# Optimization experiments

Measured on AMD Instinct MI355X. Metric: run time of the kernel, lower is better.

## Reference

```python
import jax, jax.numpy as jnp
import numpy as np

H1 = 768
H2 = 768
B, LQ, LK = 8, 1024, 1024


def setup_inputs() -> dict:
    key = jax.random.key(0)
    ks = jax.random.split(key, 12)
    s1 = 1.0 / np.sqrt(H1)
    s2 = 1.0 / np.sqrt(H2)
    # weights stored as [in, out] (equivalent to torch Linear weight.T)
    return {
        "tensor1": jax.random.normal(ks[0], (B, LQ, H1), jnp.float32),
        "tensor2": jax.random.normal(ks[1], (B, LK, H2), jnp.float32),
        "Wq": jax.random.uniform(ks[2], (3, H1, H2), jnp.float32, -s1, s1),
        "bq": jax.random.uniform(ks[3], (3, H2), jnp.float32, -s1, s1),
        "Wk": jax.random.uniform(ks[4], (3, H2, H2), jnp.float32, -s2, s2),
        "bk": jax.random.uniform(ks[5], (3, H2), jnp.float32, -s2, s2),
        "Wv": jax.random.uniform(ks[6], (3, H2, H2), jnp.float32, -s2, s2),
        "bv": jax.random.uniform(ks[7], (3, H2), jnp.float32, -s2, s2),
        "Wp": jax.random.uniform(ks[8], (3 * H2, H2), jnp.float32, -1.0 / np.sqrt(3 * H2), 1.0 / np.sqrt(3 * H2)),
        "bp": jax.random.uniform(ks[9], (H2,), jnp.float32, -1.0 / np.sqrt(3 * H2), 1.0 / np.sqrt(3 * H2)),
    }


def reference(tensor1, tensor2, Wq, bq, Wk, bk, Wv, bv, Wp, bp):
    # Three independent cross-attention heads, stacked on leading axis h=3.
    q = jnp.einsum("bqd,hde->hbqe", tensor1, Wq) + bq[:, None, None, :]  # [3,B,LQ,H2]
    k = jnp.einsum("bkd,hde->hbke", tensor2, Wk) + bk[:, None, None, :]  # [3,B,LK,H2]
    v = jnp.einsum("bkd,hde->hbke", tensor2, Wv) + bv[:, None, None, :]  # [3,B,LK,H2]
    scores = jnp.einsum("hbqe,hbke->hbqk", q, k)  # NOTE: no 1/sqrt(d) scaling, per original
    weights = jax.nn.softmax(scores, axis=-1)
    ctx = jnp.einsum("hbqk,hbke->hbqe", weights, v)  # [3,B,LQ,H2]
    # concat heads along feature dim -> [B,LQ,3*H2]
    multi = jnp.transpose(ctx, (1, 2, 0, 3)).reshape(ctx.shape[1], ctx.shape[2], -1)
    # project_multihead: ReLU then Linear
    return jax.nn.relu(multi) @ Wp + bp
```

## Files before the change

### kernel.cpp

```cpp
#include <hip/hip_runtime.h>
#include <hip/hip_bf16.h>


typedef _Float16 f16;
typedef __attribute__((ext_vector_type(8))) _Float16 f16x8;
typedef __attribute__((ext_vector_type(4))) float f32x4;
typedef __attribute__((ext_vector_type(4))) short s16x4;
typedef __attribute__((ext_vector_type(8))) short s16x8;

#define DI __device__ __forceinline__

DI short f2hs(float f){
  f16 h = (f16)f;
  return __builtin_bit_cast(short, h);
}

DI f32x4 mfma16(f16x8 a, f16x8 b, f32x4 c){
  return __builtin_amdgcn_mfma_f32_16x16x32_f16(a, b, c, 0, 0, 0);
}

#define GLL16(gp, lp) __builtin_amdgcn_global_load_lds( \
    (const __attribute__((address_space(1))) unsigned int*)(gp), \
    (__attribute__((address_space(3))) unsigned int*)(lp), 16, 0, 0)

__global__ void pre_fused_kernel(
    const float* __restrict__ t1, const float* __restrict__ t2,
    short* __restrict__ t1b, short* __restrict__ t2b,
    const float* __restrict__ Wq, const float* __restrict__ Wk,
    short* __restrict__ Mt,
    const float* __restrict__ Wv, const float* __restrict__ Wp,
    short* __restrict__ WvT, short* __restrict__ WpT,
    const float* __restrict__ bq, float* __restrict__ wvb)
{
  __shared__ short As[8192];
  __shared__ short Bs[8192];
  __shared__ float tile[32][33];
  int bid = blockIdx.x;
  const int tid = threadIdx.x;

  if (bid < 108){
    const int h = bid / 36, rem = bid % 36;
    const int m0 = (rem / 6) * 128, n0 = (rem % 6) * 128;
    const float* A  = Wq + (long)h*768*768;
    const float* Bt = Wk + (long)h*768*768;
    const int wave = tid>>6, lane = tid&63;
    const int wm = wave>>1, wn = wave&1;
    const int fl = lane&15, fq = lane>>4;
    const int srow = lane>>2, sl = lane&3;
    const int gco = (sl ^ ((srow>>1)&3))*8;
    const int rs  = (fq ^ ((fl>>1)&3))*8;

    f32x4 vz = {0.f,0.f,0.f,0.f};
    f32x4 acc[4][4];
    #pragma unroll
    for (int i=0;i<4;i++)
      #pragma unroll
      for (int j=0;j<4;j++) acc[i][j] = vz;

    for (int kk=0; kk<768; kk+=64){
      __syncthreads();
      #pragma unroll
      for (int c=0;c<2;c++)
        #pragma unroll
        for (int r=0;r<2;r++){
          const int row = r*64 + wave*16 + srow;
          const int gc  = kk + c*32 + gco;
          const float* pa = A  + (long)(m0+row)*768 + gc;
          const float* pb = Bt + (long)(n0+row)*768 + gc;
          f32x4 a0 = *(const f32x4*)pa, a1 = *(const f32x4*)(pa+4);
          f32x4 b0 = *(const f32x4*)pb, b1 = *(const f32x4*)(pb+4);
          s16x8 ha, hb;
          #pragma unroll
          for (int e=0;e<4;e++){ ha[e]=f2hs(a0[e]); ha[4+e]=f2hs(a1[e]);
                                 hb[e]=f2hs(b0[e]); hb[4+e]=f2hs(b1[e]); }
          *(s16x8*)(As + c*4096 + row*32 + sl*8) = ha;
          *(s16x8*)(Bs + c*4096 + row*32 + sl*8) = hb;
        }
      __syncthreads();
      #pragma unroll
      for (int c=0;c<2;c++){
        f16x8 a[4];
        #pragma unroll
        for (int i=0;i<4;i++) a[i] = *(const f16x8*)(As + c*4096 + (wm*64+i*16+fl)*32 + rs);
        #pragma unroll
        for (int j=0;j<4;j++){
          f16x8 b = *(const f16x8*)(Bs + c*4096 + (wn*64+j*16+fl)*32 + rs);
          #pragma unroll
          for (int i=0;i<4;i++) acc[i][j] = mfma16(a[i], b, acc[i][j]);
        }
      }
    }

    short* outp = Mt + (long)h*768*768;
    #pragma unroll
    for (int j=0;j<4;j++){
      int col = n0 + wn*64 + j*16 + fl;
      #pragma unroll
      for (int i=0;i<4;i++){
        int row = m0 + wm*64 + i*16 + fq*4;
        s16x4 pack;
        #pragma unroll
        for (int r=0;r<4;r++) pack[r] = f2hs(acc[i][j][r]);
        *(s16x4*)(outp + (long)col*768 + row) = pack;
      }
    }
    return;
  }
  bid -= 108;
  if (bid < 24){
    const int h = bid / 8, chunk = bid % 8;
    const int wave = tid>>6, lane = tid&63;
    const float* bql = bq + h*768 + lane*12;
    float bv[12];
    #pragma unroll
    for (int e=0;e<12;e++) bv[e] = bql[e];
    for (int r = 0; r < 24; r++){
      int d = chunk*96 + r*4 + wave;
      const float* row = Wk + ((long)h*768 + d)*768 + lane*12;
      float s = 0.f;
      #pragma unroll
      for (int e=0;e<12;e++) s += row[e] * bv[e];
      s += __shfl_xor(s, 1);
      s += __shfl_xor(s, 2);
      s += __shfl_xor(s, 4);
      s += __shfl_xor(s, 8);
      s += __shfl_xor(s, 16);
      s += __shfl_xor(s, 32);
      if (lane == 0) wvb[h*768 + d] = s;
    }
    return;
  }
  bid -= 24;
  if (bid < 3456){
    const int bz = bid / 1728, rem = bid % 1728;
    const int by = rem / 24, bx = rem % 24;
    const float* in; short* out; int R, r0;
    if (bz == 0){
      int hd = by / 24;
      in = Wv + (long)hd*768*768; out = WvT + (long)hd*768*768;
      R = 768; r0 = (by % 24) * 32;
    } else {
      in = Wp; out = WpT; R = 2304; r0 = by * 32;
    }
    int c0 = bx * 32;
    int tx = tid & 31, ty = tid >> 5;
    #pragma unroll
    for (int k=0;k<4;k++)
      tile[ty + k*8][tx] = in[(long)(r0 + ty + k*8) * 768 + c0 + tx];
    __syncthreads();
    #pragma unroll
    for (int k=0;k<4;k++)
      out[(long)(c0 + ty + k*8) * R + r0 + tx] = f2hs(tile[tx][ty + k*8]);
    return;
  }
  bid -= 3456;
  {
    int i = bid*256 + tid;
    const float* in = (i < 1572864) ? t1 : t2;
    short* out = (i < 1572864) ? t1b : t2b;
    int j = (i < 1572864) ? i : i - 1572864;
    f32x4 v = ((const f32x4*)in)[j];
    s16x4 o;
    o[0]=f2hs(v[0]); o[1]=f2hs(v[1]); o[2]=f2hs(v[2]); o[3]=f2hs(v[3]);
    ((s16x4*)out)[j] = o;
  }
}

DI void gemm_tile64(const short* __restrict__ A, const short* __restrict__ Bt, int K,
                    int m0, int n0, short* As, short* Bs, f32x4 (&acc)[4][4])
{
  const int tid = threadIdx.x, wave = tid>>6, lane = tid&63;
  const int wm = wave>>1, wn = wave&1;
  const int fl = lane&15, fq = lane>>4;
  const int srow = lane>>2;
  const int scol = ((lane&3) ^ ((lane>>3)&3))*8;
  const int rs   = (fq ^ ((fl>>1)&3))*8;
  for (int kk=0; kk<K; kk+=64){
    __syncthreads();
    #pragma unroll
    for (int c=0;c<2;c++)
      #pragma unroll
      for (int r=0;r<2;r++){
        const int rb = r*64 + wave*16;
        GLL16(A  + (long)(m0+rb+srow)*K + kk + c*32 + scol, As + c*4096 + rb*32);
        GLL16(Bt + (long)(n0+rb+srow)*K + kk + c*32 + scol, Bs + c*4096 + rb*32);
      }
    __syncthreads();
    #pragma unroll
    for (int c=0;c<2;c++){
      f16x8 a[4];
      #pragma unroll
      for (int i=0;i<4;i++) a[i] = *(const f16x8*)(As + c*4096 + (wm*64+i*16+fl)*32 + rs);
      #pragma unroll
      for (int j=0;j<4;j++){
        f16x8 b = *(const f16x8*)(Bs + c*4096 + (wn*64+j*16+fl)*32 + rs);
        #pragma unroll
        for (int i=0;i<4;i++) acc[i][j] = mfma16(a[i], b, acc[i][j]);
      }
    }
  }
}

__global__ __launch_bounds__(256,2) void gemm_gv_kernel(
    const short* __restrict__ t1b, const short* __restrict__ t2b,
    const short* __restrict__ Mt, const short* __restrict__ WvT,
    const float* __restrict__ wv, const float* __restrict__ bv,
    short* __restrict__ Gb, short* __restrict__ Vtb)
{
  __shared__ short As[8192];
  __shared__ short Bs[8192];
  const int z = blockIdx.z;
  const int h = z % 3, which = z / 3;
  const short* A  = (which==0) ? t1b : t2b;
  const short* Bt = ((which==0)?Mt:WvT) + (long)h*768*768;
  const int m0 = blockIdx.x*128, n0 = blockIdx.y*128;
  const int tid = threadIdx.x, wave = tid>>6, lane = tid&63;
  const int wm = wave>>1, wn = wave&1;
  const int fl = lane&15, fq = lane>>4;

  f32x4 vz = {0.f,0.f,0.f,0.f};
  f32x4 acc[4][4];
  #pragma unroll
  for (int i=0;i<4;i++)
    #pragma unroll
    for (int j=0;j<4;j++) acc[i][j] = vz;

  gemm_tile64(A, Bt, 768, m0, n0, As, Bs, acc);

  if (which == 0){
    const float* bias = wv + h*768;
    short* outp = Gb + (long)h*8192*768;
    #pragma unroll
    for (int j=0;j<4;j++){
      int col = n0 + wn*64 + j*16 + fl;
      float bb = bias[col];
      #pragma unroll
      for (int i=0;i<4;i++){
        int row = m0 + wm*64 + i*16 + fq*4;
        #pragma unroll
        for (int r=0;r<4;r++)
          outp[(long)(row+r)*768 + col] = f2hs(acc[i][j][r] + bb);
      }
    }
  } else {
    const float* bias = bv + h*768;
    const int bidx = m0 >> 10;
    const int lk0  = m0 & 1023;
    short* outp = Vtb + (long)(h*8 + bidx)*768*1024;
    #pragma unroll
    for (int j=0;j<4;j++){
      int e = n0 + wn*64 + j*16 + fl;
      float bb = bias[e];
      #pragma unroll
      for (int i=0;i<4;i++){
        int lk = lk0 + wm*64 + i*16 + fq*4;
        s16x4 pack;
        #pragma unroll
        for (int r=0;r<4;r++) pack[r] = f2hs(acc[i][j][r] + bb);
        *(s16x4*)(outp + (long)e*1024 + lk) = pack;
      }
    }
  }
}

__global__ __launch_bounds__(256,2) void qk_exp_kernel(
    const short* __restrict__ Gb, const short* __restrict__ t2b,
    short* __restrict__ P, float* __restrict__ Mx, float* __restrict__ Lx)
{
  __shared__ short As[8192];
  __shared__ short Bs[8192];
  __shared__ float red0[2][2][64];
  __shared__ float red1[2][2][64];
  const int id = blockIdx.x;
  const int xcd = id & 7, s_ = id >> 3;
  const int hb = xcd*3 + (s_ >> 6);
  const int inner = s_ & 63;
  const int qt = inner & 7, ct = inner >> 3;
  const int h = hb >> 3, b = hb & 7;
  const int tid = threadIdx.x, wave = tid>>6, lane = tid&63;
  const int wm = wave>>1, wn = wave&1;
  const int fl = lane&15, fq = lane>>4;
  const short* Abase = Gb + ((long)h*8192 + b*1024)*768;
  const short* Bbase = t2b + (long)b*1024*768;

  f32x4 vz = {0.f,0.f,0.f,0.f};
  f32x4 acc[4][4];
  #pragma unroll
  for (int i=0;i<4;i++)
    #pragma unroll
    for (int j=0;j<4;j++) acc[i][j] = vz;

  gemm_tile64(Abase, Bbase, 768, qt*128, ct*128, As, Bs, acc);

  float mt[4][4];
  #pragma unroll
  for (int i=0;i<4;i++)
    #pragma unroll
    for (int r=0;r<4;r++){
      float m = acc[i][0][r];
      #pragma unroll
      for (int j=1;j<4;j++) m = fmaxf(m, acc[i][j][r]);
      m = fmaxf(m, __shfl_xor(m, 1));
      m = fmaxf(m, __shfl_xor(m, 2));
      m = fmaxf(m, __shfl_xor(m, 4));
      m = fmaxf(m, __shfl_xor(m, 8));
      mt[i][r] = m;
      if (fl == 0) red0[wn][wm][i*16 + fq*4 + r] = m;
    }
  __syncthreads();
  #pragma unroll
  for (int i=0;i<4;i++)
    #pragma unroll
    for (int r=0;r<4;r++)
      mt[i][r] = fmaxf(red0[0][wm][i*16 + fq*4 + r], red0[1][wm][i*16 + fq*4 + r]);

  #pragma unroll
  for (int i=0;i<4;i++)
    #pragma unroll
    for (int r=0;r<4;r++){
      float s = 0.f;
      #pragma unroll
      for (int j=0;j<4;j++){
        float p = __expf(acc[i][j][r] - mt[i][r]);
        acc[i][j][r] = p;
        s += p;
      }
      s += __shfl_xor(s, 1);
      s += __shfl_xor(s, 2);
      s += __shfl_xor(s, 4);
      s += __shfl_xor(s, 8);
      if (fl == 0) red1[wn][wm][i*16 + fq*4 + r] = s;
    }
  __syncthreads();

  #pragma unroll
  for (int j=0;j<4;j++){
    int c = ct*128 + wn*64 + j*16 + fl;
    #pragma unroll
    for (int i=0;i<4;i++){
      int q = qt*128 + wm*64 + i*16 + fq*4;
      #pragma unroll
      for (int r=0;r<4;r++)
        P[((long)hb*1024 + q + r)*1024 + c] = f2hs(acc[i][j][r]);
    }
  }
  if (fl == 0 && wn == 0){
    long aux = ((long)(hb*8 + ct))*1024 + qt*128;
    #pragma unroll
    for (int i=0;i<4;i++)
      #pragma unroll
      for (int r=0;r<4;r++){
        int row = wm*64 + i*16 + fq*4 + r;
        Mx[aux + row] = mt[i][r];
        Lx[aux + row] = red1[0][wm][row & 63] + red1[1][wm][row & 63];
      }
  }
}

__global__ __launch_bounds__(256,2) void pv_kernel(
    const short* __restrict__ P, const short* __restrict__ Vtb,
    const float* __restrict__ Mx, const float* __restrict__ Lx, short* __restrict__ multi)
{
  __shared__ short As[8192];
  __shared__ short Bs[8192];
  __shared__ float scl[8][128];
  const int id = blockIdx.x;
  const int xcd = id & 7, s_ = id >> 3;
  const int hb = xcd*3 + s_/48;
  const int inner = s_ % 48;
  const int qt = inner & 7, et = inner >> 3;
  const int h = hb >> 3, b = hb & 7;
  const int tid = threadIdx.x, wave = tid>>6, lane = tid&63;
  const int wm = wave>>1, wn = wave&1;
  const int fl = lane&15, fq = lane>>4;
  const int srow = lane>>2;
  const int scol = ((lane&3) ^ ((lane>>3)&3))*8;
  const int rs   = (fq ^ ((fl>>1)&3))*8;
  const short* Abase = P + (long)hb*1024*1024 + (long)(qt*128)*1024;
  const short* Bbase = Vtb + (long)hb*768*1024 + (long)(et*128)*1024;

  if (tid < 128){
    long a0 = ((long)(hb*8))*1024 + qt*128 + tid;
    float m[8], l[8];
    #pragma unroll
    for (int t=0;t<8;t++){ m[t] = Mx[a0 + t*1024]; l[t] = Lx[a0 + t*1024]; }
    float mg = m[0];
    #pragma unroll
    for (int t=1;t<8;t++) mg = fmaxf(mg, m[t]);
    float lg = 0.f;
    #pragma unroll
    for (int t=0;t<8;t++) lg += l[t] * __expf(m[t] - mg);
    float inv = 1.0f / lg;
    #pragma unroll
    for (int t=0;t<8;t++) scl[t][tid] = __expf(m[t] - mg) * inv;
  }
  __syncthreads();

  f32x4 vz = {0.f,0.f,0.f,0.f};
  f32x4 acc[4][4];
  #pragma unroll
  for (int i=0;i<4;i++)
    #pragma unroll
    for (int j=0;j<4;j++) acc[i][j] = vz;

  for (int ct=0; ct<8; ct++){
    f16 s[4];
    #pragma unroll
    for (int i=0;i<4;i++) s[i] = (f16)scl[ct][wm*64 + i*16 + fl];
    #pragma unroll
    for (int t=0;t<2;t++){
      const int kk = ct*128 + t*64;
      __syncthreads();
      #pragma unroll
      for (int c=0;c<2;c++)
        #pragma unroll
        for (int r=0;r<2;r++){
          const int rb = r*64 + wave*16;
          GLL16(Abase + (long)(rb+srow)*1024 + kk + c*32 + scol, As + c*4096 + rb*32);
          GLL16(Bbase + (long)(rb+srow)*1024 + kk + c*32 + scol, Bs + c*4096 + rb*32);
        }
      __syncthreads();
      #pragma unroll
      for (int c=0;c<2;c++){
        f16x8 a[4];
        #pragma unroll
        for (int i=0;i<4;i++){
          f16x8 av = *(const f16x8*)(As + c*4096 + (wm*64+i*16+fl)*32 + rs);
          f16x8 sv;
          #pragma unroll
          for (int e=0;e<8;e++) sv[e] = s[i];
          a[i] = av * sv;
        }
        #pragma unroll
        for (int j=0;j<4;j++){
          f16x8 bvv = *(const f16x8*)(Bs + c*4096 + (wn*64+j*16+fl)*32 + rs);
          #pragma unroll
          for (int i=0;i<4;i++) acc[i][j] = mfma16(a[i], bvv, acc[i][j]);
        }
      }
    }
  }

  short* mp = multi + (long)(b*1024 + qt*128)*2304 + h*768 + et*128;
  #pragma unroll
  for (int j=0;j<4;j++){
    int e = wn*64 + j*16 + fl;
    #pragma unroll
    for (int i=0;i<4;i++){
      int q = wm*64 + i*16 + fq*4;
      #pragma unroll
      for (int r=0;r<4;r++)
        mp[(long)(q+r)*2304 + e] = f2hs(fmaxf(acc[i][j][r], 0.f));
    }
  }
}

__global__ __launch_bounds__(256,2) void gemm_out_kernel(
    const short* __restrict__ A, const short* __restrict__ Bt,
    const float* __restrict__ bias, float* __restrict__ out)
{
  __shared__ short As[8192];
  __shared__ short Bs[8192];
  const int m0 = blockIdx.x*128, n0 = blockIdx.y*128;
  const int tid = threadIdx.x, wave = tid>>6, lane = tid&63;
  const int wm = wave>>1, wn = wave&1;
  const int fl = lane&15, fq = lane>>4;

  f32x4 vz = {0.f,0.f,0.f,0.f};
  f32x4 acc[4][4];
  #pragma unroll
  for (int i=0;i<4;i++)
    #pragma unroll
    for (int j=0;j<4;j++) acc[i][j] = vz;

  gemm_tile64(A, Bt, 2304, m0, n0, As, Bs, acc);

  #pragma unroll
  for (int j=0;j<4;j++){
    int col = n0 + wn*64 + j*16 + fl;
    float bb = bias[col];
    #pragma unroll
    for (int i=0;i<4;i++){
      int row = m0 + wm*64 + i*16 + fq*4;
      #pragma unroll
      for (int r=0;r<4;r++)
        out[(long)(row+r)*768 + col] = acc[i][j][r] + bb;
    }
  }
}

extern "C" void kernel_launch(void* const* d_in, const int* in_sizes, int n_in,
                              void* d_out, int out_size, void* d_ws, size_t ws_size,
                              hipStream_t stream)
{
  const float* t1 = (const float*)d_in[0];
  const float* t2 = (const float*)d_in[1];
  const float* Wq = (const float*)d_in[2];
  const float* bq = (const float*)d_in[3];
  const float* Wk = (const float*)d_in[4];
  const float* Wv = (const float*)d_in[6];
  const float* bv = (const float*)d_in[7];
  const float* Wp = (const float*)d_in[8];
  const float* bp = (const float*)d_in[9];
  float* out = (float*)d_out;

  char* ws = (char*)d_ws;
  size_t off = 0;
  auto carve = [&](size_t bytes){ void* p = ws + off; off += (bytes + 255) & ~(size_t)255; return p; };
  short* t1b = (short*)carve(8L*1024*768*2);
  short* t2b = (short*)carve(8L*1024*768*2);
  short* WvT = (short*)carve(3L*768*768*2);
  short* WpT = (short*)carve(768L*2304*2);
  short* Mt  = (short*)carve(3L*768*768*2);
  short* Gb  = (short*)carve(3L*8192*768*2);
  short* Vtb = (short*)carve(3L*8*768*1024*2);
  short* Pb  = (short*)carve(24L*1024*1024*2);
  float* Mx  = (float*)carve(24L*8*1024*4);
  float* Lx  = (float*)carve(24L*8*1024*4);
  float* wvb = (float*)carve(3L*768*4);
  short* multib = Gb;

  pre_fused_kernel<<<15876, 256, 0, stream>>>(t1, t2, t1b, t2b, Wq, Wk, Mt,
                                              Wv, Wp, WvT, WpT, bq, wvb);
  gemm_gv_kernel<<<dim3(64,6,6), 256, 0, stream>>>(t1b, t2b, Mt, WvT, wvb, bv, Gb, Vtb);
  qk_exp_kernel<<<1536, 256, 0, stream>>>(Gb, t2b, Pb, Mx, Lx);
  pv_kernel<<<1152, 256, 0, stream>>>(Pb, Vtb, Mx, Lx, multib);
  gemm_out_kernel<<<dim3(64,6,1), 256, 0, stream>>>(multib, WpT, bp, out);
}
```

Before: 364.4 us.

## Enlarge QK and PV block tiles to 256-wide with 8-wave blocks

The QK-exp kernel now uses 512-thread blocks covering 256 query rows by 128 key columns, with an inline K-loop in place of the shared gemm_tile64 helper. The PV kernel now covers 128 query rows by 256 output features with 8 waves. Both grids are halved accordingly. The intent is to reuse each loaded B or A tile across more rows and cut redundant global loads. In exchange, each block uses more LDS, and the launch bounds of 4 blocks of 512 threads may be unachievable or raise register pressure.

```diff
diff --git a/kernel.cpp b/kernel.cpp
--- a/kernel.cpp
+++ b/kernel.cpp
@@ -263,25 +263,28 @@
   }
 }
 
-__global__ __launch_bounds__(256,2) void qk_exp_kernel(
+__global__ __launch_bounds__(512,4) void qk_exp_kernel(
     const short* __restrict__ Gb, const short* __restrict__ t2b,
     short* __restrict__ P, float* __restrict__ Mx, float* __restrict__ Lx)
 {
-  __shared__ short As[8192];
+  __shared__ short As[16384];
   __shared__ short Bs[8192];
-  __shared__ float red0[2][2][64];
-  __shared__ float red1[2][2][64];
+  __shared__ float red0[2][4][64];
+  __shared__ float red1[2][4][64];
   const int id = blockIdx.x;
   const int xcd = id & 7, s_ = id >> 3;
-  const int hb = xcd*3 + (s_ >> 6);
-  const int inner = s_ & 63;
-  const int qt = inner & 7, ct = inner >> 3;
+  const int hb = xcd*3 + (s_ >> 5);
+  const int inner = s_ & 31;
+  const int qt = inner & 3, ct = inner >> 2;
   const int h = hb >> 3, b = hb & 7;
   const int tid = threadIdx.x, wave = tid>>6, lane = tid&63;
-  const int wm = wave>>1, wn = wave&1;
+  const int wq = wave>>1, wc = wave&1;
   const int fl = lane&15, fq = lane>>4;
-  const short* Abase = Gb + ((long)h*8192 + b*1024)*768;
-  const short* Bbase = t2b + (long)b*1024*768;
+  const int srow = lane>>2;
+  const int scol = ((lane&3) ^ ((lane>>3)&3))*8;
+  const int rs   = (fq ^ ((fl>>1)&3))*8;
+  const short* Abase = Gb + ((long)h*8192 + b*1024 + qt*256)*768;
+  const short* Bbase = t2b + ((long)b*1024 + ct*128)*768;
 
   f32x4 vz = {0.f,0.f,0.f,0.f};
   f32x4 acc[4][4];
@@ -290,7 +293,32 @@
     #pragma unroll
     for (int j=0;j<4;j++) acc[i][j] = vz;
 
-  gemm_tile64(Abase, Bbase, 768, qt*128, ct*128, As, Bs, acc);
+  for (int kk=0; kk<768; kk+=64){
+    __syncthreads();
+    #pragma unroll
+    for (int c=0;c<2;c++){
+      #pragma unroll
+      for (int r=0;r<2;r++){
+        const int rb = r*128 + wave*16;
+        GLL16(Abase + (long)(rb+srow)*768 + kk + c*32 + scol, As + c*8192 + rb*32);
+      }
+      const int rbB = wave*16;
+      GLL16(Bbase + (long)(rbB+srow)*768 + kk + c*32 + scol, Bs + c*4096 + rbB*32);
+    }
+    __syncthreads();
+    #pragma unroll
+    for (int c=0;c<2;c++){
+      f16x8 a[4];
+      #pragma unroll
+      for (int i=0;i<4;i++) a[i] = *(const f16x8*)(As + c*8192 + (wq*64+i*16+fl)*32 + rs);
+      #pragma unroll
+      for (int j=0;j<4;j++){
+        f16x8 bfr = *(const f16x8*)(Bs + c*4096 + (wc*64+j*16+fl)*32 + rs);
+        #pragma unroll
+        for (int i=0;i<4;i++) acc[i][j] = mfma16(a[i], bfr, acc[i][j]);
+      }
+    }
+  }
 
   float mt[4][4];
   #pragma unroll
@@ -305,14 +333,14 @@
       m = fmaxf(m, __shfl_xor(m, 4));
       m = fmaxf(m, __shfl_xor(m, 8));
       mt[i][r] = m;
-      if (fl == 0) red0[wn][wm][i*16 + fq*4 + r] = m;
+      if (fl == 0) red0[wc][wq][i*16 + fq*4 + r] = m;
     }
   __syncthreads();
   #pragma unroll
   for (int i=0;i<4;i++)
     #pragma unroll
     for (int r=0;r<4;r++)
-      mt[i][r] = fmaxf(red0[0][wm][i*16 + fq*4 + r], red0[1][wm][i*16 + fq*4 + r]);
+      mt[i][r] = fmaxf(red0[0][wq][i*16 + fq*4 + r], red0[1][wq][i*16 + fq*4 + r]);
 
   #pragma unroll
   for (int i=0;i<4;i++)
@@ -329,55 +357,55 @@
       s += __shfl_xor(s, 2);
       s += __shfl_xor(s, 4);
       s += __shfl_xor(s, 8);
-      if (fl == 0) red1[wn][wm][i*16 + fq*4 + r] = s;
+      if (fl == 0) red1[wc][wq][i*16 + fq*4 + r] = s;
     }
   __syncthreads();
 
   #pragma unroll
   for (int j=0;j<4;j++){
-    int c = ct*128 + wn*64 + j*16 + fl;
+    int c = ct*128 + wc*64 + j*16 + fl;
     #pragma unroll
     for (int i=0;i<4;i++){
-      int q = qt*128 + wm*64 + i*16 + fq*4;
+      int q = qt*256 + wq*64 + i*16 + fq*4;
       #pragma unroll
       for (int r=0;r<4;r++)
         P[((long)hb*1024 + q + r)*1024 + c] = f2hs(acc[i][j][r]);
     }
   }
-  if (fl == 0 && wn == 0){
-    long aux = ((long)(hb*8 + ct))*1024 + qt*128;
+  if (fl == 0 && wc == 0){
+    long aux = ((long)(hb*8 + ct))*1024 + qt*256;
     #pragma unroll
     for (int i=0;i<4;i++)
       #pragma unroll
       for (int r=0;r<4;r++){
-        int row = wm*64 + i*16 + fq*4 + r;
+        int row = wq*64 + i*16 + fq*4 + r;
         Mx[aux + row] = mt[i][r];
-        Lx[aux + row] = red1[0][wm][row & 63] + red1[1][wm][row & 63];
-      }
-  }
-}
-
-__global__ __launch_bounds__(256,2) void pv_kernel(
+        Lx[aux + row] = red1[0][wq][row & 63] + red1[1][wq][row & 63];
+      }
+  }
+}
+
+__global__ __launch_bounds__(512,4) void pv_kernel(
     const short* __restrict__ P, const short* __restrict__ Vtb,
     const float* __restrict__ Mx, const float* __restrict__ Lx, short* __restrict__ multi)
 {
   __shared__ short As[8192];
-  __shared__ short Bs[8192];
+  __shared__ short Bs[16384];
   __shared__ float scl[8][128];
   const int id = blockIdx.x;
   const int xcd = id & 7, s_ = id >> 3;
-  const int hb = xcd*3 + s_/48;
-  const int inner = s_ % 48;
-  const int qt = inner & 7, et = inner >> 3;
+  const int hb = xcd*3 + s_/24;
+  const int inner = s_ % 24;
+  const int qt = inner & 7, eg = inner >> 3;
   const int h = hb >> 3, b = hb & 7;
   const int tid = threadIdx.x, wave = tid>>6, lane = tid&63;
-  const int wm = wave>>1, wn = wave&1;
+  const int wm = wave>>2, wn = wave&3;
   const int fl = lane&15, fq = lane>>4;
   const int srow = lane>>2;
   const int scol = ((lane&3) ^ ((lane>>3)&3))*8;
   const int rs   = (fq ^ ((fl>>1)&3))*8;
   const short* Abase = P + (long)hb*1024*1024 + (long)(qt*128)*1024;
-  const short* Bbase = Vtb + (long)hb*768*1024 + (long)(et*128)*1024;
+  const short* Bbase = Vtb + (long)hb*768*1024 + (long)(eg*256)*1024;
 
   if (tid < 128){
     long a0 = ((long)(hb*8))*1024 + qt*128 + tid;
@@ -412,13 +440,15 @@
       const int kk = ct*128 + t*64;
       __syncthreads();
       #pragma unroll
-      for (int c=0;c<2;c++)
+      for (int c=0;c<2;c++){
+        const int rbA = wave*16;
+        GLL16(Abase + (long)(rbA+srow)*1024 + kk + c*32 + scol, As + c*4096 + rbA*32);
         #pragma unroll
         for (int r=0;r<2;r++){
-          const int rb = r*64 + wave*16;
-          GLL16(Abase + (long)(rb+srow)*1024 + kk + c*32 + scol, As + c*4096 + rb*32);
-          GLL16(Bbase + (long)(rb+srow)*1024 + kk + c*32 + scol, Bs + c*4096 + rb*32);
+          const int rb = r*128 + wave*16;
+          GLL16(Bbase + (long)(rb+srow)*1024 + kk + c*32 + scol, Bs + c*8192 + rb*32);
         }
+      }
       __syncthreads();
       #pragma unroll
       for (int c=0;c<2;c++){
@@ -433,7 +463,7 @@
         }
         #pragma unroll
         for (int j=0;j<4;j++){
-          f16x8 bvv = *(const f16x8*)(Bs + c*4096 + (wn*64+j*16+fl)*32 + rs);
+          f16x8 bvv = *(const f16x8*)(Bs + c*8192 + (wn*64+j*16+fl)*32 + rs);
           #pragma unroll
           for (int i=0;i<4;i++) acc[i][j] = mfma16(a[i], bvv, acc[i][j]);
         }
@@ -441,7 +471,7 @@
     }
   }
 
-  short* mp = multi + (long)(b*1024 + qt*128)*2304 + h*768 + et*128;
+  short* mp = multi + (long)(b*1024 + qt*128)*2304 + h*768 + eg*256;
   #pragma unroll
   for (int j=0;j<4;j++){
     int e = wn*64 + j*16 + fl;
@@ -523,7 +553,7 @@
   pre_fused_kernel<<<15876, 256, 0, stream>>>(t1, t2, t1b, t2b, Wq, Wk, Mt,
                                               Wv, Wp, WvT, WpT, bq, wvb);
   gemm_gv_kernel<<<dim3(64,6,6), 256, 0, stream>>>(t1b, t2b, Mt, WvT, wvb, bv, Gb, Vtb);
-  qk_exp_kernel<<<1536, 256, 0, stream>>>(Gb, t2b, Pb, Mx, Lx);
-  pv_kernel<<<1152, 256, 0, stream>>>(Pb, Vtb, Mx, Lx, multib);
+  qk_exp_kernel<<<768, 512, 0, stream>>>(Gb, t2b, Pb, Mx, Lx);
+  pv_kernel<<<576, 512, 0, stream>>>(Pb, Vtb, Mx, Lx, multib);
   gemm_out_kernel<<<dim3(64,6,1), 256, 0, stream>>>(multib, WpT, bp, out);
 }
```

After: 391.2 us. +7.3%, slower.
